# Performance work log

Measured on AMD Instinct MI355X. Metric: run time of the kernel, lower is better.

Reference implementation:

```python
import jax, jax.numpy as jnp
import numpy as np

N_EXPERTS = 8
TOP_K = 2
D_MODEL = 1024
D_INNER = 4096
BATCH = 8
SEQ = 2048


def setup_inputs() -> dict:
    key = jax.random.key(0)
    k_x, k_g, k_e = jax.random.split(key, 3)
    sequences = jax.random.normal(k_x, (BATCH, SEQ, D_MODEL), dtype=jnp.float32)
    # gating Linear(d_model -> n_experts)
    gating_w = jax.random.normal(k_g, (N_EXPERTS, D_MODEL), dtype=jnp.float32) * (1.0 / np.sqrt(D_MODEL))
    gating_b = jnp.zeros((N_EXPERTS,), dtype=jnp.float32)
    # expert Linear(d_model -> d_inner), xavier_uniform
    xav = float(np.sqrt(6.0 / (D_MODEL + D_INNER)))
    expert_w = jax.random.uniform(k_e, (N_EXPERTS, D_INNER, D_MODEL), dtype=jnp.float32, minval=-xav, maxval=xav)
    expert_b = jnp.zeros((N_EXPERTS, D_INNER), dtype=jnp.float32)
    return {"sequences": sequences, "gating_w": gating_w, "gating_b": gating_b,
            "expert_w": expert_w, "expert_b": expert_b}


def reference(sequences, gating_w, gating_b, expert_w, expert_b):
    N, P, D = sequences.shape
    x = sequences.reshape(N * P, D)                                  # [T, D]
    gating_scores = jax.nn.softmax(x @ gating_w.T + gating_b, axis=-1)  # [T, E]
    _, top_k_indices = jax.lax.top_k(gating_scores, TOP_K)          # [T, K]
    # mask[t, e] = expert e is among token t's top-k (indices are distinct)
    mask = (top_k_indices[:, :, None] == jnp.arange(N_EXPERTS)[None, None, :]).any(axis=1)  # [T, E]
    maskf = mask.astype(x.dtype)
    out = jnp.zeros((N * P, D_INNER), dtype=x.dtype)
    for e in range(N_EXPERTS):  # small fixed expert count
        out = out + maskf[:, e:e + 1] * (x @ expert_w[e].T + expert_b[e])
    out = out / TOP_K
    # training-mode auxiliary: per-expert variance of gating scores (unbiased, like torch.var)
    gating_variances = jnp.var(gating_scores, axis=0, ddof=1)        # [E]
    return out.reshape(N, P, D_INNER), gating_variances
```

## Files before the change

kernel.cpp:

```cpp
#include <hip/hip_runtime.h>

#define T_TOKENS 16384
#define DM 1024
#define DI 4096
#define NE 8
#define PAIRS 64
#define CAP 16384

typedef float f32x4 __attribute__((ext_vector_type(4)));
typedef __bf16 bf16x8 __attribute__((ext_vector_type(8)));

__device__ inline unsigned short f2b(float f) {
  union { float f; unsigned u; } v; v.f = f;
  unsigned r = v.u + 0x7FFFu + ((v.u >> 16) & 1u);
  return (unsigned short)(r >> 16);
}

__global__ __launch_bounds__(256) void k_gating(
    const float* __restrict__ x, const float* __restrict__ gw, const float* __restrict__ gb,
    unsigned short* __restrict__ x16, float* __restrict__ scores,
    int* __restrict__ cnt, int* __restrict__ ptok)
{
  int wid  = (blockIdx.x * 256 + threadIdx.x) >> 6;
  int lane = threadIdx.x & 63;
  if (wid >= T_TOKENS) return;
  const float* xr = x + (size_t)wid * DM;

  double acc[NE];
  #pragma unroll
  for (int e = 0; e < NE; e++) acc[e] = 0.0;

  #pragma unroll
  for (int u = 0; u < 4; u++) {
    int off = u * 256 + lane * 4;
    float4 xv = *(const float4*)(xr + off);
    ushort4 pk; pk.x = f2b(xv.x); pk.y = f2b(xv.y); pk.z = f2b(xv.z); pk.w = f2b(xv.w);
    *(ushort4*)(x16 + (size_t)wid * DM + off) = pk;
    #pragma unroll
    for (int e = 0; e < NE; e++) {
      float4 wv = *(const float4*)(gw + e * DM + off);
      acc[e] += (double)xv.x * wv.x + (double)xv.y * wv.y
              + (double)xv.z * wv.z + (double)xv.w * wv.w;
    }
  }
  #pragma unroll
  for (int e = 0; e < NE; e++) {
    double v = acc[e];
    #pragma unroll
    for (int s = 32; s > 0; s >>= 1) v += __shfl_xor(v, s, 64);
    acc[e] = v + (double)gb[e];
  }
  if (lane == 0) {
    double m = acc[0];
    for (int e = 1; e < NE; e++) if (acc[e] > m) m = acc[e];
    double ex[NE], sum = 0.0;
    for (int e = 0; e < NE; e++) { ex[e] = exp(acc[e] - m); sum += ex[e]; }
    double inv = 1.0 / sum;
    for (int e = 0; e < NE; e++) scores[(size_t)wid * NE + e] = (float)(ex[e] * inv);
    int e1 = 0; double b1 = acc[0];
    for (int e = 1; e < NE; e++) if (acc[e] > b1) { b1 = acc[e]; e1 = e; }
    int e2 = -1; double b2 = -1e300;
    for (int e = 0; e < NE; e++) if (e != e1 && acc[e] > b2) { b2 = acc[e]; e2 = e; }
    int lo = e1 < e2 ? e1 : e2, hi = e1 < e2 ? e2 : e1;
    int p = lo * 8 + hi;
    int pos = atomicAdd(&cnt[p], 1);
    ptok[p * CAP + pos] = wid;
  }
}

__global__ __launch_bounds__(256) void k_wconv(const float* __restrict__ w, unsigned short* __restrict__ w16) {
  size_t i = ((size_t)blockIdx.x * 256 + threadIdx.x) * 4;
  float4 v = *(const float4*)(w + i);
  ushort4 pk; pk.x = f2b(v.x); pk.y = f2b(v.y); pk.z = f2b(v.z); pk.w = f2b(v.w);
  *(ushort4*)(w16 + i) = pk;
}

__global__ void k_sched(const int* __restrict__ cnt, int* __restrict__ tiles, int* __restrict__ ntiles) {
  if (threadIdx.x == 0 && blockIdx.x == 0) {
    int n = 0;
    for (int p = 0; p < PAIRS; p++) {
      int c = cnt[p];
      for (int r = 0; r < c; r += 128) { tiles[2 * n] = p; tiles[2 * n + 1] = r; n++; }
    }
    *ntiles = n;
  }
}

__global__ __launch_bounds__(256) void k_gemm(
    const unsigned short* __restrict__ x16, const unsigned short* __restrict__ w16,
    const float* __restrict__ eb, const int* __restrict__ cnt,
    const int* __restrict__ ptok, const int* __restrict__ tiles, const int* __restrict__ ntiles,
    float* __restrict__ out)
{
  __shared__ unsigned short As[128 * 64];
  __shared__ unsigned short Bs[2][128 * 64];

  int tileIdx = blockIdx.y;
  if (tileIdx >= *ntiles) return;
  int p    = tiles[2 * tileIdx];
  int row0 = tiles[2 * tileIdx + 1];
  int e1 = p >> 3, e2 = p & 7;
  int c  = cnt[p];
  int nTile = blockIdx.x;
  int tid  = threadIdx.x;
  int lane = tid & 63;
  int wid  = tid >> 6;
  int waveM = wid >> 1, waveN = wid & 1;

  int tok[4];
  #pragma unroll
  for (int i = 0; i < 4; i++) {
    int rg = row0 + (tid >> 3) + i * 32;
    if (rg > c - 1) rg = c - 1;
    tok[i] = ptok[p * CAP + rg];
  }
  int kc = (tid & 7) * 8;

  f32x4 acc[4][4];
  #pragma unroll
  for (int i = 0; i < 4; i++)
    #pragma unroll
    for (int j = 0; j < 4; j++) acc[i][j] = {0.f, 0.f, 0.f, 0.f};

  const unsigned short* bb1 = w16 + ((size_t)e1 * DI + (size_t)nTile * 128) * DM;
  const unsigned short* bb2 = w16 + ((size_t)e2 * DI + (size_t)nTile * 128) * DM;

  for (int k0 = 0; k0 < DM; k0 += 64) {
    #pragma unroll
    for (int i = 0; i < 4; i++) {
      int r = (tid >> 3) + i * 32;
      __builtin_amdgcn_global_load_lds(
          (const __attribute__((address_space(1))) void*)(x16 + (size_t)tok[i] * DM + k0 + kc),
          (__attribute__((address_space(3))) void*)(&As[r * 64 + kc]), 16, 0, 0);
      __builtin_amdgcn_global_load_lds(
          (const __attribute__((address_space(1))) void*)(bb1 + (size_t)r * DM + k0 + kc),
          (__attribute__((address_space(3))) void*)(&Bs[0][r * 64 + kc]), 16, 0, 0);
      __builtin_amdgcn_global_load_lds(
          (const __attribute__((address_space(1))) void*)(bb2 + (size_t)r * DM + k0 + kc),
          (__attribute__((address_space(3))) void*)(&Bs[1][r * 64 + kc]), 16, 0, 0);
    }
    __syncthreads();
    #pragma unroll
    for (int kk = 0; kk < 2; kk++) {
      int ko = kk * 32 + (lane >> 4) * 8;
      bf16x8 af[4], bf0[4], bf1[4];
      #pragma unroll
      for (int mi = 0; mi < 4; mi++)
        af[mi] = *(const bf16x8*)&As[(waveM * 64 + mi * 16 + (lane & 15)) * 64 + ko];
      #pragma unroll
      for (int ni = 0; ni < 4; ni++) {
        bf0[ni] = *(const bf16x8*)&Bs[0][(waveN * 64 + ni * 16 + (lane & 15)) * 64 + ko];
        bf1[ni] = *(const bf16x8*)&Bs[1][(waveN * 64 + ni * 16 + (lane & 15)) * 64 + ko];
      }
      #pragma unroll
      for (int mi = 0; mi < 4; mi++)
        #pragma unroll
        for (int ni = 0; ni < 4; ni++) {
          acc[mi][ni] = __builtin_amdgcn_mfma_f32_16x16x32_bf16(af[mi], bf0[ni], acc[mi][ni], 0, 0, 0);
          acc[mi][ni] = __builtin_amdgcn_mfma_f32_16x16x32_bf16(af[mi], bf1[ni], acc[mi][ni], 0, 0, 0);
        }
    }
    __syncthreads();
  }

  int colbase = nTile * 128 + waveN * 64;
  float bsum[4];
  #pragma unroll
  for (int ni = 0; ni < 4; ni++) {
    int col = colbase + ni * 16 + (lane & 15);
    bsum[ni] = 0.5f * (eb[e1 * DI + col] + eb[e2 * DI + col]);
  }
  #pragma unroll
  for (int mi = 0; mi < 4; mi++) {
    #pragma unroll
    for (int r2 = 0; r2 < 4; r2++) {
      int row = waveM * 64 + mi * 16 + (lane >> 4) * 4 + r2;
      int rg = row0 + row;
      if (rg < c) {
        int t = ptok[p * CAP + rg];
        float* orow = out + (size_t)t * DI + colbase;
        #pragma unroll
        for (int ni = 0; ni < 4; ni++)
          orow[ni * 16 + (lane & 15)] = 0.5f * acc[mi][ni][r2] + bsum[ni];
      }
    }
  }
}

__global__ __launch_bounds__(256) void k_var(const float* __restrict__ scores, float* __restrict__ vout) {
  int e = blockIdx.x, tid = threadIdx.x;
  double s = 0.0, s2 = 0.0;
  for (int t = tid; t < T_TOKENS; t += 256) {
    double v = (double)scores[(size_t)t * NE + e];
    s += v; s2 += v * v;
  }
  __shared__ double ls[256], ls2[256];
  ls[tid] = s; ls2[tid] = s2; __syncthreads();
  for (int st = 128; st > 0; st >>= 1) {
    if (tid < st) { ls[tid] += ls[tid + st]; ls2[tid] += ls2[tid + st]; }
    __syncthreads();
  }
  if (tid == 0) {
    double mean = ls[0] / (double)T_TOKENS;
    vout[e] = (float)((ls2[0] - ls[0] * mean) / (double)(T_TOKENS - 1));
  }
}

extern "C" void kernel_launch(void* const* d_in, const int* in_sizes, int n_in,
                              void* d_out, int out_size, void* d_ws, size_t ws_size,
                              hipStream_t stream)
{
  const float* x  = (const float*)d_in[0];
  const float* gw = (const float*)d_in[1];
  const float* gb = (const float*)d_in[2];
  const float* ew = (const float*)d_in[3];
  const float* eb = (const float*)d_in[4];
  float* out = (float*)d_out;

  char* ws = (char*)d_ws;
  unsigned short* x16 = (unsigned short*)ws;
  unsigned short* w16 = (unsigned short*)(ws + 33554432);
  float* scores       = (float*)(ws + 100663296);
  int*   ptok         = (int*)(ws + 101187584);
  int*   cnt          = (int*)(ws + 105381888);
  int*   ntiles       = (int*)(ws + 105382144);
  int*   tiles        = (int*)(ws + 105382160);

  hipMemsetAsync(cnt, 0, PAIRS * sizeof(int), stream);
  k_gating<<<dim3(4096), dim3(256), 0, stream>>>(x, gw, gb, x16, scores, cnt, ptok);
  k_wconv <<<dim3(32768), dim3(256), 0, stream>>>(ew, w16);
  k_sched <<<dim3(1), dim3(64), 0, stream>>>(cnt, tiles, ntiles);
  k_gemm  <<<dim3(32, 160), dim3(256), 0, stream>>>(x16, w16, eb, cnt, ptok, tiles, ntiles, out);
  k_var   <<<dim3(8), dim3(256), 0, stream>>>(scores, out + 67108864);
}
```

Before: 856.6 us.

## Swizzle LDS tiles in MoE GEMM, parallelize tile scheduling, widen weight conversion

Result: faster. 829.0 us (-3.2%).

```diff
diff --git a/kernel.cpp b/kernel.cpp
--- a/kernel.cpp
+++ b/kernel.cpp
@@ -69,21 +69,29 @@
 }
 
 __global__ __launch_bounds__(256) void k_wconv(const float* __restrict__ w, unsigned short* __restrict__ w16) {
-  size_t i = ((size_t)blockIdx.x * 256 + threadIdx.x) * 4;
-  float4 v = *(const float4*)(w + i);
-  ushort4 pk; pk.x = f2b(v.x); pk.y = f2b(v.y); pk.z = f2b(v.z); pk.w = f2b(v.w);
-  *(ushort4*)(w16 + i) = pk;
+  size_t i = ((size_t)blockIdx.x * 256 + threadIdx.x) * 8;
+  float4 a = *(const float4*)(w + i);
+  float4 b = *(const float4*)(w + i + 4);
+  ushort4 pa, pb;
+  pa.x = f2b(a.x); pa.y = f2b(a.y); pa.z = f2b(a.z); pa.w = f2b(a.w);
+  pb.x = f2b(b.x); pb.y = f2b(b.y); pb.z = f2b(b.z); pb.w = f2b(b.w);
+  *(ushort4*)(w16 + i) = pa;
+  *(ushort4*)(w16 + i + 4) = pb;
 }
 
 __global__ void k_sched(const int* __restrict__ cnt, int* __restrict__ tiles, int* __restrict__ ntiles) {
-  if (threadIdx.x == 0 && blockIdx.x == 0) {
-    int n = 0;
-    for (int p = 0; p < PAIRS; p++) {
-      int c = cnt[p];
-      for (int r = 0; r < c; r += 128) { tiles[2 * n] = p; tiles[2 * n + 1] = r; n++; }
-    }
-    *ntiles = n;
-  }
+  int p = threadIdx.x;
+  int c = cnt[p];
+  int nt = (c + 127) >> 7;
+  int inc = nt;
+  #pragma unroll
+  for (int s = 1; s < 64; s <<= 1) {
+    int v = __shfl_up(inc, s, 64);
+    if (p >= s) inc += v;
+  }
+  int excl = inc - nt;
+  for (int i = 0; i < nt; i++) { tiles[2 * (excl + i)] = p; tiles[2 * (excl + i) + 1] = i * 128; }
+  if (p == 63) *ntiles = inc;
 }
 
 __global__ __launch_bounds__(256) void k_gemm(
@@ -114,7 +122,6 @@
     if (rg > c - 1) rg = c - 1;
     tok[i] = ptok[p * CAP + rg];
   }
-  int kc = (tid & 7) * 8;
 
   f32x4 acc[4][4];
   #pragma unroll
@@ -128,29 +135,37 @@
   for (int k0 = 0; k0 < DM; k0 += 64) {
     #pragma unroll
     for (int i = 0; i < 4; i++) {
-      int r = (tid >> 3) + i * 32;
+      int r  = (tid >> 3) + i * 32;
+      int cS = tid & 7;
+      int kg = ((cS ^ (r & 7)) * 8);
       __builtin_amdgcn_global_load_lds(
-          (const __attribute__((address_space(1))) void*)(x16 + (size_t)tok[i] * DM + k0 + kc),
-          (__attribute__((address_space(3))) void*)(&As[r * 64 + kc]), 16, 0, 0);
+          (const __attribute__((address_space(1))) void*)(x16 + (size_t)tok[i] * DM + k0 + kg),
+          (__attribute__((address_space(3))) void*)(&As[r * 64 + cS * 8]), 16, 0, 0);
       __builtin_amdgcn_global_load_lds(
-          (const __attribute__((address_space(1))) void*)(bb1 + (size_t)r * DM + k0 + kc),
-          (__attribute__((address_space(3))) void*)(&Bs[0][r * 64 + kc]), 16, 0, 0);
+          (const __attribute__((address_space(1))) void*)(bb1 + (size_t)r * DM + k0 + kg),
+          (__attribute__((address_space(3))) void*)(&Bs[0][r * 64 + cS * 8]), 16, 0, 0);
       __builtin_amdgcn_global_load_lds(
-          (const __attribute__((address_space(1))) void*)(bb2 + (size_t)r * DM + k0 + kc),
-          (__attribute__((address_space(3))) void*)(&Bs[1][r * 64 + kc]), 16, 0, 0);
+          (const __attribute__((address_space(1))) void*)(bb2 + (size_t)r * DM + k0 + kg),
+          (__attribute__((address_space(3))) void*)(&Bs[1][r * 64 + cS * 8]), 16, 0, 0);
     }
     __syncthreads();
     #pragma unroll
     for (int kk = 0; kk < 2; kk++) {
-      int ko = kk * 32 + (lane >> 4) * 8;
+      int q  = lane >> 4;
+      int m  = lane & 15;
+      int jg = kk * 4 + q;
       bf16x8 af[4], bf0[4], bf1[4];
       #pragma unroll
-      for (int mi = 0; mi < 4; mi++)
-        af[mi] = *(const bf16x8*)&As[(waveM * 64 + mi * 16 + (lane & 15)) * 64 + ko];
+      for (int mi = 0; mi < 4; mi++) {
+        int R = waveM * 64 + mi * 16 + m;
+        af[mi] = *(const bf16x8*)&As[R * 64 + ((jg ^ (R & 7)) * 8)];
+      }
       #pragma unroll
       for (int ni = 0; ni < 4; ni++) {
-        bf0[ni] = *(const bf16x8*)&Bs[0][(waveN * 64 + ni * 16 + (lane & 15)) * 64 + ko];
-        bf1[ni] = *(const bf16x8*)&Bs[1][(waveN * 64 + ni * 16 + (lane & 15)) * 64 + ko];
+        int R = waveN * 64 + ni * 16 + m;
+        int o = R * 64 + ((jg ^ (R & 7)) * 8);
+        bf0[ni] = *(const bf16x8*)&Bs[0][o];
+        bf1[ni] = *(const bf16x8*)&Bs[1][o];
       }
       #pragma unroll
       for (int mi = 0; mi < 4; mi++)
@@ -228,7 +243,7 @@
 
   hipMemsetAsync(cnt, 0, PAIRS * sizeof(int), stream);
   k_gating<<<dim3(4096), dim3(256), 0, stream>>>(x, gw, gb, x16, scores, cnt, ptok);
-  k_wconv <<<dim3(32768), dim3(256), 0, stream>>>(ew, w16);
+  k_wconv <<<dim3(16384), dim3(256), 0, stream>>>(ew, w16);
   k_sched <<<dim3(1), dim3(64), 0, stream>>>(cnt, tiles, ntiles);
   k_gemm  <<<dim3(32, 160), dim3(256), 0, stream>>>(x16, w16, eb, cnt, ptok, tiles, ntiles, out);
   k_var   <<<dim3(8), dim3(256), 0, stream>>>(scores, out + 67108864);
```
